# Optimization experiments

Measured on AMD Instinct MI355X. Metric: run time of the kernel, lower is better.

The kernel has to match this reference:

```python
import jax, jax.numpy as jnp
import numpy as np

B, T, S = 4, 4096, 4096
D_MODEL = 512        # d_query = d_value_in = d_key_in
N_HEADS = 8
D_KEY = 512
D_VALUE = 512
N_OMEGA = 64
EPS = 1e-9
DK_H = D_KEY // N_HEADS      # 64
DV_H = D_VALUE // N_HEADS    # 64


def _glorot(key, shape):
    fan_in, fan_out = shape[-2], shape[-1]
    lim = np.sqrt(6.0 / (fan_in + fan_out))
    return jax.random.uniform(key, shape, jnp.float32, -lim, lim)


def _draw_omega(key, d_feature, n_omega):
    # n_omega == d_feature here -> single orthogonal block scaled by sqrt(d)
    g = jax.random.normal(key, (d_feature, d_feature), jnp.float32)
    q, _ = jnp.linalg.qr(g)
    q = q * jnp.sqrt(jnp.float32(d_feature))
    return q[:n_omega]


def setup_inputs() -> dict:
    key = jax.random.key(0)
    ks = jax.random.split(key, 7)
    return {
        "query": 0.5 * jax.random.normal(ks[0], (B, T, D_MODEL), jnp.float32),
        "value": 0.5 * jax.random.normal(ks[1], (B, S, D_MODEL), jnp.float32),
        "key": 0.5 * jax.random.normal(ks[2], (B, S, D_MODEL), jnp.float32),
        "wq": _glorot(ks[3], (N_HEADS, D_MODEL, DK_H)),
        "wv": _glorot(ks[4], (N_HEADS, D_MODEL, DV_H)),
        "wk": _glorot(ks[5], (N_HEADS, D_MODEL, DK_H)),
        "omega": _draw_omega(ks[6], DK_H, N_OMEGA),
    }


def _phi(x, omega):
    # x: (B,H,T,dk_h) -> (B,H,T,2*n_omega) FAVOR+ positive random features
    square_sum = 0.5 * jnp.sum(x * x, axis=-1, keepdims=True)
    xw = jnp.einsum('bhtk,mk->bhtm', x, omega)
    un = jnp.exp(jnp.concatenate([xw, -xw], axis=-1) - square_sum) + EPS
    return un / jnp.sqrt(jnp.float32(2.0 * N_OMEGA))


def reference(query, value, key, wq, wv, wk, omega):
    q = jnp.einsum('btf,hfk->bhtk', query, wq)   # (B,H,T,dk_h)
    v = jnp.einsum('bsd,hdk->bhsk', value, wv)   # (B,H,S,dv_h)
    k = jnp.einsum('bsf,hfk->bhsk', key, wk)     # (B,H,S,dk_h)
    qp = _phi(q, omega)                          # (B,H,T,2M)
    kp = _phi(k, omega)                          # (B,H,S,2M)
    v1 = jnp.concatenate([v, jnp.ones(v.shape[:-1] + (1,), v.dtype)], axis=-1)
    kv = jnp.einsum('bhsm,bhsd->bhmd', kp, v1)   # (B,H,2M,dv_h+1)
    qkv = jnp.einsum('bhtm,bhmd->bhtd', qp, kv)  # (B,H,T,dv_h+1)
    normalizer = qkv[..., -1:]
    out = qkv[..., :-1] / normalizer
    # faithful to original: plain reshape (B,H,T,dv_h) -> (B,T,D_VALUE), no transpose
    return jnp.reshape(out, (B, T, D_VALUE))
```

## Files before the change

kernel.cpp:

```cpp
#include <hip/hip_runtime.h>

typedef _Float16 half8 __attribute__((ext_vector_type(8)));
typedef _Float16 half4_t __attribute__((ext_vector_type(4)));
typedef short short8 __attribute__((ext_vector_type(8)));
typedef unsigned short u16x4 __attribute__((ext_vector_type(4)));
typedef float f32x4 __attribute__((ext_vector_type(4)));

#define NH 8

__device__ __forceinline__ unsigned short f2bf(float x) {
  union { float f; unsigned u; } v; v.f = x;
  unsigned r = v.u + 0x7FFFu + ((v.u >> 16) & 1u);
  return (unsigned short)(r >> 16);
}

#define DRAIN_BAR()                                  \
  asm volatile("s_waitcnt lgkmcnt(0)" ::: "memory"); \
  __builtin_amdgcn_s_barrier();                      \
  __builtin_amdgcn_sched_barrier(0)

__global__ __launch_bounds__(256) void k0_qk(
    const float* __restrict__ wq, const float* __restrict__ wk,
    const float* __restrict__ omega,
    _Float16* __restrict__ wxq, _Float16* __restrict__ wxk) {
  const int bid = blockIdx.x;
  const int arr = bid >> 7;
  const int h = (bid >> 4) & 7;
  const int ft = (bid >> 1) & 7;
  const int os = bid & 1;
  const int f = threadIdx.x & 63;
  const int w = threadIdx.x >> 6;
  const float* wsrc = (arr ? wk : wq) + ((size_t)h * 512 + ft * 64 + f) * 64;
  float wreg[64];
#pragma unroll
  for (int i = 0; i < 16; ++i) {
    float4 v = *(const float4*)(wsrc + i * 4);
    wreg[i * 4] = v.x; wreg[i * 4 + 1] = v.y; wreg[i * 4 + 2] = v.z; wreg[i * 4 + 3] = v.w;
  }
  _Float16* outp = arr ? wxk : wxq;
  const int k8 = f >> 3, e = f & 7;
#pragma unroll 1
  for (int oo = 0; oo < 8; ++oo) {
    const int o = w * 16 + os * 8 + oo;
    const float* om = omega + o * 64;
    float s = 0.f;
#pragma unroll
    for (int k = 0; k < 64; ++k) s = fmaf(wreg[k], om[k], s);
    outp[((((size_t)h * 8 + ft) * 8 + k8) * 64 + o) * 8 + e] = (_Float16)s;
  }
}

__global__ __launch_bounds__(256) void k0_v(
    const float* __restrict__ wv, _Float16* __restrict__ wvt) {
  int idx = blockIdx.x * 256 + threadIdx.x;
  int h = idx >> 15, o = (idx >> 9) & 63, f = idx & 511;
  float val = wv[((size_t)h * 512 + f) * 64 + o];
  wvt[((((size_t)h * 8 + (f >> 6)) * 8 + ((f >> 3) & 7)) * 64 + o) * 8 + (f & 7)] = (_Float16)val;
}

__global__ __launch_bounds__(512, 1) void fused_kv(
    const float* __restrict__ key, const float* __restrict__ value,
    const _Float16* __restrict__ wxk, const _Float16* __restrict__ wvt,
    float* __restrict__ kvpart) {
  __shared__ __align__(16) _Float16 A[2][128][72];
  __shared__ __align__(16) _Float16 W[2][2][4096];
  __shared__ __align__(16) unsigned short kpT[128][136];
  __shared__ __align__(16) unsigned short vT[64][136];
  const int bid = blockIdx.x;
  const int hp = bid >> 6;
  const int b = (bid >> 4) & 3;
  const int sc = bid & 15;
  const int s0 = sc * 256;
  const int tid = threadIdx.x;
  const int w = tid >> 6;
  const int lane = tid & 63;
  const int g = lane >> 4, c = lane & 15;
  const int hh = w >> 2;
  const int rq = w & 3;
  const int xr = lane >> 4;
  const int xc = (lane & 15) * 4;

  const _Float16* wkb0 = wxk + (size_t)(hp * 2) * 32768;
  const _Float16* wkb1 = wkb0 + 32768;
  const _Float16* wvb0 = wvt + (size_t)(hp * 2) * 32768;
  const _Float16* wvb1 = wvb0 + 32768;

  short8 bones;
#pragma unroll
  for (int i = 0; i < 8; ++i) bones[i] = (c == 0) ? (short)0x3F80 : (short)0;

  f32x4 acc_kv[2][5];
#pragma unroll
  for (int h2 = 0; h2 < 2; ++h2)
#pragma unroll
    for (int j = 0; j < 5; ++j) acc_kv[h2][j] = (f32x4){0.f, 0.f, 0.f, 0.f};

  u16x4 kps[2][4], kms[2][4], vs_[2][4];

  float4 xv[4];
  half8 wr0, wr1;

#pragma unroll 1
  for (int p = 0; p < 4; ++p) {
    const float* xb = ((p & 1) ? value : key) +
                      (size_t)(b * 4096 + s0 + (p >> 1) * 128 + w * 16 + xr) * 512 + xc;
    const _Float16* wb0 = (p & 1) ? wvb0 : wkb0;
    const _Float16* wb1 = (p & 1) ? wvb1 : wkb1;

#pragma unroll
    for (int i = 0; i < 4; ++i) xv[i] = *(const float4*)(xb + i * 2048);
    wr0 = *(const half8*)(wb0 + tid * 8);
    wr1 = *(const half8*)(wb1 + tid * 8);
#pragma unroll
    for (int i = 0; i < 4; ++i) {
      float vv[4] = {xv[i].x, xv[i].y, xv[i].z, xv[i].w};
      half4_t hv;
#pragma unroll
      for (int j2 = 0; j2 < 4; ++j2) hv[j2] = (_Float16)vv[j2];
      *(half4_t*)&A[0][w * 16 + i * 4 + xr][xc] = hv;
    }
    *(half8*)&W[0][0][tid * 8] = wr0;
    *(half8*)&W[0][1][tid * 8] = wr1;
#pragma unroll
    for (int i = 0; i < 4; ++i) xv[i] = *(const float4*)(xb + 64 + i * 2048);
    wr0 = *(const half8*)(wb0 + 4096 + tid * 8);
    wr1 = *(const half8*)(wb1 + 4096 + tid * 8);
    DRAIN_BAR();

    f32x4 accp[2][4];
#pragma unroll
    for (int mf = 0; mf < 2; ++mf)
#pragma unroll
      for (int j = 0; j < 4; ++j) accp[mf][j] = (f32x4){0.f, 0.f, 0.f, 0.f};

#pragma unroll 1
    for (int kc = 0; kc < 8; ++kc) {
      const int cur = kc & 1;
      if (kc < 7) {
        const int nxt = cur ^ 1;
#pragma unroll
        for (int i = 0; i < 4; ++i) {
          float vv[4] = {xv[i].x, xv[i].y, xv[i].z, xv[i].w};
          half4_t hv;
#pragma unroll
          for (int j2 = 0; j2 < 4; ++j2) hv[j2] = (_Float16)vv[j2];
          *(half4_t*)&A[nxt][w * 16 + i * 4 + xr][xc] = hv;
        }
        *(half8*)&W[nxt][0][tid * 8] = wr0;
        *(half8*)&W[nxt][1][tid * 8] = wr1;
        if (kc < 6) {
#pragma unroll
          for (int i = 0; i < 4; ++i)
            xv[i] = *(const float4*)(xb + (kc + 2) * 64 + i * 2048);
          wr0 = *(const half8*)(wb0 + (kc + 2) * 4096 + tid * 8);
          wr1 = *(const half8*)(wb1 + (kc + 2) * 4096 + tid * 8);
        }
      }
#pragma unroll
      for (int ks = 0; ks < 2; ++ks) {
        half8 af0 = *(const half8*)&A[cur][rq * 32 + c][ks * 32 + g * 8];
        half8 af1 = *(const half8*)&A[cur][rq * 32 + 16 + c][ks * 32 + g * 8];
#pragma unroll
        for (int nf = 0; nf < 4; ++nf) {
          half8 wf = *(const half8*)&W[cur][hh][((ks * 4 + g) * 64 + nf * 16 + c) * 8];
          accp[0][nf] = __builtin_amdgcn_mfma_f32_16x16x32_f16(af0, wf, accp[0][nf], 0, 0, 0);
          accp[1][nf] = __builtin_amdgcn_mfma_f32_16x16x32_f16(af1, wf, accp[1][nf], 0, 0, 0);
        }
      }
      DRAIN_BAR();
    }

    if ((p & 1) == 0) {
#pragma unroll
      for (int mf = 0; mf < 2; ++mf) {
        float ss_[4];
#pragma unroll
        for (int j = 0; j < 4; ++j) {
          float s = 0.f;
#pragma unroll
          for (int nf = 0; nf < 4; ++nf) { float q = accp[mf][nf][j]; s = fmaf(q, q, s); }
          s += __shfl_xor(s, 1); s += __shfl_xor(s, 2);
          s += __shfl_xor(s, 4); s += __shfl_xor(s, 8);
          ss_[j] = s * 0.0078125f;
        }
#pragma unroll
        for (int nf = 0; nf < 4; ++nf) {
          u16x4 kp_p, kp_m;
#pragma unroll
          for (int j = 0; j < 4; ++j) {
            float v = accp[mf][nf][j];
            kp_p[j] = f2bf(__expf(v - ss_[j]) + 1e-9f);
            kp_m[j] = f2bf(__expf(-v - ss_[j]) + 1e-9f);
          }
          kps[mf][nf] = kp_p;
          kms[mf][nf] = kp_m;
        }
      }
    } else {
#pragma unroll
      for (int mf = 0; mf < 2; ++mf)
#pragma unroll
        for (int nf = 0; nf < 4; ++nf) {
          u16x4 vv;
#pragma unroll
          for (int j = 0; j < 4; ++j) vv[j] = f2bf(accp[mf][nf][j]);
          vs_[mf][nf] = vv;
        }
#pragma unroll
      for (int h2 = 0; h2 < 2; ++h2) {
        if (hh == h2) {
#pragma unroll
          for (int mf = 0; mf < 2; ++mf)
#pragma unroll
            for (int nf = 0; nf < 4; ++nf) {
              const int m = nf * 16 + c;
              const int sl = rq * 32 + mf * 16 + g * 4;
              *(u16x4*)&kpT[m][sl] = kps[mf][nf];
              *(u16x4*)&kpT[64 + m][sl] = kms[mf][nf];
              *(u16x4*)&vT[m][sl] = vs_[mf][nf];
            }
        }
        DRAIN_BAR();
#pragma unroll
        for (int ks = 0; ks < 4; ++ks) {
          short8 a = *(const short8*)&kpT[w * 16 + c][ks * 32 + g * 8];
#pragma unroll
          for (int nf = 0; nf < 4; ++nf) {
            short8 bb = *(const short8*)&vT[nf * 16 + c][ks * 32 + g * 8];
            acc_kv[h2][nf] = __builtin_amdgcn_mfma_f32_16x16x32_bf16(a, bb, acc_kv[h2][nf], 0, 0, 0);
          }
          acc_kv[h2][4] = __builtin_amdgcn_mfma_f32_16x16x32_bf16(a, bones, acc_kv[h2][4], 0, 0, 0);
        }
        __builtin_amdgcn_s_barrier();
      }
    }
  }

#pragma unroll
  for (int h2 = 0; h2 < 2; ++h2) {
    float* pbase = kvpart + ((size_t)sc * 32 + b * 8 + hp * 2 + h2) * 10240;
#pragma unroll
    for (int nf = 0; nf < 5; ++nf)
#pragma unroll
      for (int j = 0; j < 4; ++j)
        pbase[(w * 16 + g * 4 + j) * 80 + nf * 16 + c] = acc_kv[h2][nf][j];
  }
}

__global__ __launch_bounds__(128) void k3a_denom(
    const float* __restrict__ kvpart, float* __restrict__ invbuf,
    float* __restrict__ lsc) {
  const int bh = blockIdx.x;
  const int m = threadIdx.x;
  const float* base = kvpart + (size_t)bh * 10240 + m * 80 + 64;
  float s = 0.f;
#pragma unroll
  for (int kk = 0; kk < 16; ++kk) s += base[(size_t)kk * 327680];
  invbuf[bh * 128 + m] = 1.0f / s;
  lsc[bh * 128 + m] = __logf(s);
}

__global__ __launch_bounds__(256) void k3b_reduce(
    const float* __restrict__ kvpart, const float* __restrict__ invbuf,
    _Float16* __restrict__ kvnt) {
  const int bh = blockIdx.x;
  const int e0 = blockIdx.y * 1024 + threadIdx.x * 4;
  const int m = e0 / 80;
  const int d0 = e0 - m * 80;
  const float* base = kvpart + (size_t)bh * 10240 + e0;
  f32x4 s = (f32x4){0.f, 0.f, 0.f, 0.f};
#pragma unroll
  for (int kk = 0; kk < 16; ++kk) {
    f32x4 v = *(const f32x4*)(base + (size_t)kk * 327680);
    s += v;
  }
  const float inv = invbuf[bh * 128 + m];
  const int mst = ((m & 63) << 1) | (m >> 6);
  _Float16* outb = kvnt + (size_t)bh * 10240 + mst;
#pragma unroll
  for (int j = 0; j < 4; ++j) {
    const int d = d0 + j;
    float val;
    if (d < 64) val = s[j] * inv;
    else if (d == 64) val = 1.0f;
    else val = 0.f;
    outb[d * 128] = (_Float16)val;
  }
}

__global__ __launch_bounds__(256, 4) void fused_qo(
    const float* __restrict__ query, const _Float16* __restrict__ wxq,
    const _Float16* __restrict__ kvnt, const float* __restrict__ lsc,
    float* __restrict__ out) {
  __shared__ __align__(16) _Float16 A[64][72];
  __shared__ __align__(16) _Float16 W[4096];
  __shared__ __align__(16) _Float16 qpT[64][136];
  const int bid = blockIdx.x;
  const int h = bid >> 8;
  const int rt = bid & 255;
  const int R0 = rt * 64;
  const int b = R0 >> 12;
  const int t0 = R0 & 4095;
  const int bh = b * NH + h;
  const int tid = threadIdx.x;
  const int w = tid >> 6;
  const int lane = tid & 63;
  const int g = lane >> 4, c = lane & 15;
  const int srow = tid >> 2;
  const int scol = (tid & 3) * 16;

  const float* xb = query + (size_t)(R0 + srow) * 512 + scol;
  const _Float16* wb = wxq + (size_t)h * 32768;

  float4 xv[4];
  half8 wr0, wr1;
#pragma unroll
  for (int i = 0; i < 4; ++i) xv[i] = *(const float4*)(xb + i * 4);
  wr0 = *(const half8*)(wb + tid * 8);
  wr1 = *(const half8*)(wb + 2048 + tid * 8);

  f32x4 accp[4];
#pragma unroll
  for (int j = 0; j < 4; ++j) accp[j] = (f32x4){0.f, 0.f, 0.f, 0.f};

#pragma unroll 1
  for (int kc = 0; kc < 8; ++kc) {
    DRAIN_BAR();
#pragma unroll
    for (int i = 0; i < 4; ++i) {
      float vv[4] = {xv[i].x, xv[i].y, xv[i].z, xv[i].w};
      half4_t hv;
#pragma unroll
      for (int j2 = 0; j2 < 4; ++j2) hv[j2] = (_Float16)vv[j2];
      *(half4_t*)&A[srow][scol + i * 4] = hv;
    }
    *(half8*)&W[tid * 8] = wr0;
    *(half8*)&W[2048 + tid * 8] = wr1;
    if (kc < 7) {
#pragma unroll
      for (int i = 0; i < 4; ++i)
        xv[i] = *(const float4*)(xb + (kc + 1) * 64 + i * 4);
      wr0 = *(const half8*)(wb + (size_t)(kc + 1) * 4096 + tid * 8);
      wr1 = *(const half8*)(wb + (size_t)(kc + 1) * 4096 + 2048 + tid * 8);
    }
    DRAIN_BAR();
#pragma unroll
    for (int ks = 0; ks < 2; ++ks) {
      half8 a = *(const half8*)&A[w * 16 + c][ks * 32 + g * 8];
#pragma unroll
      for (int nf = 0; nf < 4; ++nf) {
        half8 wf = *(const half8*)&W[((ks * 4 + g) * 64 + nf * 16 + c) * 8];
        accp[nf] = __builtin_amdgcn_mfma_f32_16x16x32_f16(a, wf, accp[nf], 0, 0, 0);
      }
    }
  }

  float Lp[4], Lm[4];
#pragma unroll
  for (int nf = 0; nf < 4; ++nf) {
    Lp[nf] = lsc[bh * 128 + nf * 16 + c];
    Lm[nf] = lsc[bh * 128 + 64 + nf * 16 + c];
  }
  float ss_[4], cm_[4];
#pragma unroll
  for (int j = 0; j < 4; ++j) {
    float s = 0.f;
#pragma unroll
    for (int nf = 0; nf < 4; ++nf) { float q = accp[nf][j]; s = fmaf(q, q, s); }
    s += __shfl_xor(s, 1); s += __shfl_xor(s, 2);
    s += __shfl_xor(s, 4); s += __shfl_xor(s, 8);
    ss_[j] = s * 0.0078125f;
  }
#pragma unroll
  for (int j = 0; j < 4; ++j) {
    float m0 = -1e30f;
#pragma unroll
    for (int nf = 0; nf < 4; ++nf) {
      float v = accp[nf][j];
      m0 = fmaxf(m0, fmaxf(v - ss_[j] + Lp[nf], -v - ss_[j] + Lm[nf]));
      m0 = fmaxf(m0, fmaxf(Lp[nf], Lm[nf]) - 20.723265f);
    }
    m0 = fmaxf(m0, __shfl_xor(m0, 1)); m0 = fmaxf(m0, __shfl_xor(m0, 2));
    m0 = fmaxf(m0, __shfl_xor(m0, 4)); m0 = fmaxf(m0, __shfl_xor(m0, 8));
    cm_[j] = m0;
  }
#pragma unroll
  for (int nf = 0; nf < 4; ++nf) {
    const int m = nf * 16 + c;
#pragma unroll
    for (int j = 0; j < 4; ++j) {
      float v = accp[nf][j];
      _Float16 pp = (_Float16)(__expf(v - ss_[j] + Lp[nf] - cm_[j]) +
                               1e-9f * __expf(Lp[nf] - cm_[j]));
      _Float16 pm = (_Float16)(__expf(-v - ss_[j] + Lm[nf] - cm_[j]) +
                               1e-9f * __expf(Lm[nf] - cm_[j]));
      union { unsigned u; _Float16 hh[2]; } pk;
      pk.hh[0] = pp; pk.hh[1] = pm;
      *(unsigned*)&qpT[w * 16 + g * 4 + j][2 * m] = pk.u;
    }
  }
  DRAIN_BAR();

  f32x4 acco[5];
#pragma unroll
  for (int j = 0; j < 5; ++j) acco[j] = (f32x4){0.f, 0.f, 0.f, 0.f};
  const _Float16* kvb = kvnt + (size_t)bh * 10240;
#pragma unroll
  for (int ks = 0; ks < 4; ++ks) {
    half8 a = *(const half8*)&qpT[w * 16 + c][ks * 32 + g * 8];
#pragma unroll
    for (int nf = 0; nf < 5; ++nf) {
      half8 bb = *(const half8*)(kvb + (size_t)(nf * 16 + c) * 128 + ks * 32 + g * 8);
      acco[nf] = __builtin_amdgcn_mfma_f32_16x16x32_f16(a, bb, acco[nf], 0, 0, 0);
    }
  }
  const int tb = t0 + w * 16 + g * 4;
#pragma unroll
  for (int j = 0; j < 4; ++j) {
    float nrm = __shfl(acco[4][j], (lane & 48));
    float invn = 1.0f / nrm;
#pragma unroll
    for (int nf = 0; nf < 4; ++nf) {
      out[((size_t)bh * 4096 + tb + j) * 64 + nf * 16 + c] = acco[nf][j] * invn;
    }
  }
}

extern "C" void kernel_launch(void* const* d_in, const int* in_sizes, int n_in,
                              void* d_out, int out_size, void* d_ws, size_t ws_size,
                              hipStream_t stream) {
  const float* query = (const float*)d_in[0];
  const float* value = (const float*)d_in[1];
  const float* key   = (const float*)d_in[2];
  const float* wq    = (const float*)d_in[3];
  const float* wv    = (const float*)d_in[4];
  const float* wk    = (const float*)d_in[5];
  const float* omega = (const float*)d_in[6];
  float* out = (float*)d_out;
  char* ws = (char*)d_ws;

  _Float16* wxq  = (_Float16*)(ws);
  _Float16* wxk  = (_Float16*)(ws + 524288);
  _Float16* wvt  = (_Float16*)(ws + 1048576);
  float* kvpart  = (float*)(ws + 1572864);
  _Float16* kvnt = (_Float16*)(ws + 22544384);
  float* lsc     = (float*)(ws + 23199744);
  float* invbuf  = (float*)(ws + 23216128);

  k0_qk<<<256, 256, 0, stream>>>(wq, wk, omega, wxq, wxk);
  k0_v<<<1024, 256, 0, stream>>>(wv, wvt);
  fused_kv<<<256, 512, 0, stream>>>(key, value, wxk, wvt, kvpart);
  k3a_denom<<<32, 128, 0, stream>>>(kvpart, invbuf, lsc);
  k3b_reduce<<<dim3(32, 10), 256, 0, stream>>>(kvpart, invbuf, kvnt);
  fused_qo<<<2048, 256, 0, stream>>>(query, wxq, kvnt, lsc, out);
}
```

Measured before the change: 110.0 us.

## Process four heads per query tile in fused_qo to reuse query loads

Each fused_qo block now computes projections, feature maps and outputs for four heads of one 64-row query tile, so each query tile is read from global memory and converted to fp16 once instead of once per head. The full 256-column half of the query row block is staged in LDS, and projection-weight slices are double-buffered in LDS with register prefetch. The grid shrinks from 2048 to 512 blocks and occupancy is relaxed to 2 blocks per CU. The trade-off is less parallelism, more serial work per block, more LDS per block, and synchronous (non-prefetched) query loads for most of each tile.

```diff
diff --git a/kernel.cpp b/kernel.cpp
--- a/kernel.cpp
+++ b/kernel.cpp
@@ -288,141 +288,189 @@
   }
 }
 
-__global__ __launch_bounds__(256, 4) void fused_qo(
+__global__ __launch_bounds__(256, 2) void fused_qo(
     const float* __restrict__ query, const _Float16* __restrict__ wxq,
     const _Float16* __restrict__ kvnt, const float* __restrict__ lsc,
     float* __restrict__ out) {
-  __shared__ __align__(16) _Float16 A[64][72];
-  __shared__ __align__(16) _Float16 W[4096];
+  __shared__ __align__(16) _Float16 A[64][264];
+  __shared__ __align__(16) _Float16 W[2][4096];
   __shared__ __align__(16) _Float16 qpT[64][136];
   const int bid = blockIdx.x;
-  const int h = bid >> 8;
-  const int rt = bid & 255;
-  const int R0 = rt * 64;
-  const int b = R0 >> 12;
-  const int t0 = R0 & 4095;
-  const int bh = b * NH + h;
+  const int hh2 = bid >> 8;
+  const int b = (bid >> 6) & 3;
+  const int tt = bid & 63;
+  const int t0 = tt * 64;
   const int tid = threadIdx.x;
   const int w = tid >> 6;
   const int lane = tid & 63;
   const int g = lane >> 4, c = lane & 15;
-  const int srow = tid >> 2;
-  const int scol = (tid & 3) * 16;
-
-  const float* xb = query + (size_t)(R0 + srow) * 512 + scol;
-  const _Float16* wb = wxq + (size_t)h * 32768;
+  const int arow = tid >> 2;
+  const int ac4 = (tid & 3) * 16;
+
+  const float* xrow = query + (size_t)(b * 4096 + t0 + arow) * 512 + ac4;
+  const _Float16* wbase = wxq;
+
+  f32x4 accp[4][4];
+#pragma unroll
+  for (int h = 0; h < 4; ++h)
+#pragma unroll
+    for (int j = 0; j < 4; ++j) accp[h][j] = (f32x4){0.f, 0.f, 0.f, 0.f};
 
   float4 xv[4];
   half8 wr0, wr1;
-#pragma unroll
-  for (int i = 0; i < 4; ++i) xv[i] = *(const float4*)(xb + i * 4);
-  wr0 = *(const half8*)(wb + tid * 8);
-  wr1 = *(const half8*)(wb + 2048 + tid * 8);
-
-  f32x4 accp[4];
-#pragma unroll
-  for (int j = 0; j < 4; ++j) accp[j] = (f32x4){0.f, 0.f, 0.f, 0.f};
-
-#pragma unroll 1
-  for (int kc = 0; kc < 8; ++kc) {
+
+#pragma unroll
+  for (int i = 0; i < 4; ++i) xv[i] = *(const float4*)(xrow + i * 64);
+
+#pragma unroll
+  for (int kh = 0; kh < 2; ++kh) {
+#pragma unroll
+    for (int i = 0; i < 4; ++i) {
+      float4 v0 = xv[i];
+      half4_t hv;
+      hv[0] = (_Float16)v0.x; hv[1] = (_Float16)v0.y;
+      hv[2] = (_Float16)v0.z; hv[3] = (_Float16)v0.w;
+      *(half4_t*)&A[arow][ac4 + i * 4] = hv;
+    }
+#pragma unroll
+    for (int i = 0; i < 4; ++i) {
+      float4 v0 = xv[i];
+      half4_t hv;
+      hv[0] = (_Float16)v0.x; hv[1] = (_Float16)v0.y;
+      hv[2] = (_Float16)v0.z; hv[3] = (_Float16)v0.w;
+      *(half4_t*)&A[arow][ac4 + i * 64] = hv;
+    }
+#pragma unroll
+    for (int i = 0; i < 4; ++i) {
+#pragma unroll
+      for (int q2 = 1; q2 < 4; ++q2) {
+        float4 v = *(const float4*)(xrow + kh * 256 + i * 64 + q2 * 4);
+        half4_t hv;
+        hv[0] = (_Float16)v.x; hv[1] = (_Float16)v.y;
+        hv[2] = (_Float16)v.z; hv[3] = (_Float16)v.w;
+        *(half4_t*)&A[arow][ac4 + i * 64 + q2 * 4] = hv;
+      }
+    }
+    {
+      const _Float16* wsl0 = wbase + ((size_t)(hh2 * 4 + 0) * 8 + kh * 4 + 0) * 4096;
+      wr0 = *(const half8*)(wsl0 + tid * 8);
+      wr1 = *(const half8*)(wsl0 + 2048 + tid * 8);
+      *(half8*)&W[0][tid * 8] = wr0;
+      *(half8*)&W[0][2048 + tid * 8] = wr1;
+      const _Float16* wsl1 = wbase + ((size_t)(hh2 * 4 + 0) * 8 + kh * 4 + 1) * 4096;
+      wr0 = *(const half8*)(wsl1 + tid * 8);
+      wr1 = *(const half8*)(wsl1 + 2048 + tid * 8);
+    }
     DRAIN_BAR();
-#pragma unroll
-    for (int i = 0; i < 4; ++i) {
-      float vv[4] = {xv[i].x, xv[i].y, xv[i].z, xv[i].w};
-      half4_t hv;
-#pragma unroll
-      for (int j2 = 0; j2 < 4; ++j2) hv[j2] = (_Float16)vv[j2];
-      *(half4_t*)&A[srow][scol + i * 4] = hv;
-    }
-    *(half8*)&W[tid * 8] = wr0;
-    *(half8*)&W[2048 + tid * 8] = wr1;
-    if (kc < 7) {
-#pragma unroll
-      for (int i = 0; i < 4; ++i)
-        xv[i] = *(const float4*)(xb + (kc + 1) * 64 + i * 4);
-      wr0 = *(const half8*)(wb + (size_t)(kc + 1) * 4096 + tid * 8);
-      wr1 = *(const half8*)(wb + (size_t)(kc + 1) * 4096 + 2048 + tid * 8);
+    if (kh == 0) {
+#pragma unroll
+      for (int i = 0; i < 4; ++i) xv[i] = *(const float4*)(xrow + 256 + i * 64);
+    }
+
+#pragma unroll
+    for (int h = 0; h < 4; ++h) {
+#pragma unroll
+      for (int kc = 0; kc < 4; ++kc) {
+        const int s = h * 4 + kc;
+        const int cur = s & 1;
+        if (s < 15) {
+          *(half8*)&W[cur ^ 1][tid * 8] = wr0;
+          *(half8*)&W[cur ^ 1][2048 + tid * 8] = wr1;
+        }
+        if (s < 14) {
+          const int sn = s + 2;
+          const _Float16* wsl = wbase +
+              ((size_t)(hh2 * 4 + (sn >> 2)) * 8 + kh * 4 + (sn & 3)) * 4096;
+          wr0 = *(const half8*)(wsl + tid * 8);
+          wr1 = *(const half8*)(wsl + 2048 + tid * 8);
+        }
+#pragma unroll
+        for (int ks = 0; ks < 2; ++ks) {
+          half8 a = *(const half8*)&A[w * 16 + c][kc * 64 + ks * 32 + g * 8];
+#pragma unroll
+          for (int nf = 0; nf < 4; ++nf) {
+            half8 wf = *(const half8*)&W[cur][((ks * 4 + g) * 64 + nf * 16 + c) * 8];
+            accp[h][nf] = __builtin_amdgcn_mfma_f32_16x16x32_f16(a, wf, accp[h][nf], 0, 0, 0);
+          }
+        }
+        DRAIN_BAR();
+      }
+    }
+  }
+
+#pragma unroll
+  for (int h = 0; h < 4; ++h) {
+    const int bh = b * NH + hh2 * 4 + h;
+    float Lp[4], Lm[4];
+#pragma unroll
+    for (int nf = 0; nf < 4; ++nf) {
+      Lp[nf] = lsc[bh * 128 + nf * 16 + c];
+      Lm[nf] = lsc[bh * 128 + 64 + nf * 16 + c];
+    }
+    float ss_[4], cm_[4];
+#pragma unroll
+    for (int j = 0; j < 4; ++j) {
+      float s = 0.f;
+#pragma unroll
+      for (int nf = 0; nf < 4; ++nf) { float q = accp[h][nf][j]; s = fmaf(q, q, s); }
+      s += __shfl_xor(s, 1); s += __shfl_xor(s, 2);
+      s += __shfl_xor(s, 4); s += __shfl_xor(s, 8);
+      ss_[j] = s * 0.0078125f;
+    }
+#pragma unroll
+    for (int j = 0; j < 4; ++j) {
+      float m0 = -1e30f;
+#pragma unroll
+      for (int nf = 0; nf < 4; ++nf) {
+        float v = accp[h][nf][j];
+        m0 = fmaxf(m0, fmaxf(v - ss_[j] + Lp[nf], -v - ss_[j] + Lm[nf]));
+        m0 = fmaxf(m0, fmaxf(Lp[nf], Lm[nf]) - 20.723265f);
+      }
+      m0 = fmaxf(m0, __shfl_xor(m0, 1)); m0 = fmaxf(m0, __shfl_xor(m0, 2));
+      m0 = fmaxf(m0, __shfl_xor(m0, 4)); m0 = fmaxf(m0, __shfl_xor(m0, 8));
+      cm_[j] = m0;
+    }
+#pragma unroll
+    for (int nf = 0; nf < 4; ++nf) {
+      const int m = nf * 16 + c;
+#pragma unroll
+      for (int j = 0; j < 4; ++j) {
+        float v = accp[h][nf][j];
+        _Float16 pp = (_Float16)(__expf(v - ss_[j] + Lp[nf] - cm_[j]) +
+                                 1e-9f * __expf(Lp[nf] - cm_[j]));
+        _Float16 pm = (_Float16)(__expf(-v - ss_[j] + Lm[nf] - cm_[j]) +
+                                 1e-9f * __expf(Lm[nf] - cm_[j]));
+        union { unsigned u; _Float16 hh_[2]; } pk;
+        pk.hh_[0] = pp; pk.hh_[1] = pm;
+        *(unsigned*)&qpT[w * 16 + g * 4 + j][2 * m] = pk.u;
+      }
     }
     DRAIN_BAR();
-#pragma unroll
-    for (int ks = 0; ks < 2; ++ks) {
-      half8 a = *(const half8*)&A[w * 16 + c][ks * 32 + g * 8];
+
+    f32x4 acco[5];
+#pragma unroll
+    for (int j = 0; j < 5; ++j) acco[j] = (f32x4){0.f, 0.f, 0.f, 0.f};
+    const _Float16* kvb = kvnt + (size_t)bh * 10240;
+#pragma unroll
+    for (int ks = 0; ks < 4; ++ks) {
+      half8 a = *(const half8*)&qpT[w * 16 + c][ks * 32 + g * 8];
+#pragma unroll
+      for (int nf = 0; nf < 5; ++nf) {
+        half8 bb = *(const half8*)(kvb + (size_t)(nf * 16 + c) * 128 + ks * 32 + g * 8);
+        acco[nf] = __builtin_amdgcn_mfma_f32_16x16x32_f16(a, bb, acco[nf], 0, 0, 0);
+      }
+    }
+    const int tb = t0 + w * 16 + g * 4;
+#pragma unroll
+    for (int j = 0; j < 4; ++j) {
+      float nrm = __shfl(acco[4][j], (lane & 48));
+      float invn = 1.0f / nrm;
 #pragma unroll
       for (int nf = 0; nf < 4; ++nf) {
-        half8 wf = *(const half8*)&W[((ks * 4 + g) * 64 + nf * 16 + c) * 8];
-        accp[nf] = __builtin_amdgcn_mfma_f32_16x16x32_f16(a, wf, accp[nf], 0, 0, 0);
-      }
-    }
-  }
-
-  float Lp[4], Lm[4];
-#pragma unroll
-  for (int nf = 0; nf < 4; ++nf) {
-    Lp[nf] = lsc[bh * 128 + nf * 16 + c];
-    Lm[nf] = lsc[bh * 128 + 64 + nf * 16 + c];
-  }
-  float ss_[4], cm_[4];
-#pragma unroll
-  for (int j = 0; j < 4; ++j) {
-    float s = 0.f;
-#pragma unroll
-    for (int nf = 0; nf < 4; ++nf) { float q = accp[nf][j]; s = fmaf(q, q, s); }
-    s += __shfl_xor(s, 1); s += __shfl_xor(s, 2);
-    s += __shfl_xor(s, 4); s += __shfl_xor(s, 8);
-    ss_[j] = s * 0.0078125f;
-  }
-#pragma unroll
-  for (int j = 0; j < 4; ++j) {
-    float m0 = -1e30f;
-#pragma unroll
-    for (int nf = 0; nf < 4; ++nf) {
-      float v = accp[nf][j];
-      m0 = fmaxf(m0, fmaxf(v - ss_[j] + Lp[nf], -v - ss_[j] + Lm[nf]));
-      m0 = fmaxf(m0, fmaxf(Lp[nf], Lm[nf]) - 20.723265f);
-    }
-    m0 = fmaxf(m0, __shfl_xor(m0, 1)); m0 = fmaxf(m0, __shfl_xor(m0, 2));
-    m0 = fmaxf(m0, __shfl_xor(m0, 4)); m0 = fmaxf(m0, __shfl_xor(m0, 8));
-    cm_[j] = m0;
-  }
-#pragma unroll
-  for (int nf = 0; nf < 4; ++nf) {
-    const int m = nf * 16 + c;
-#pragma unroll
-    for (int j = 0; j < 4; ++j) {
-      float v = accp[nf][j];
-      _Float16 pp = (_Float16)(__expf(v - ss_[j] + Lp[nf] - cm_[j]) +
-                               1e-9f * __expf(Lp[nf] - cm_[j]));
-      _Float16 pm = (_Float16)(__expf(-v - ss_[j] + Lm[nf] - cm_[j]) +
-                               1e-9f * __expf(Lm[nf] - cm_[j]));
-      union { unsigned u; _Float16 hh[2]; } pk;
-      pk.hh[0] = pp; pk.hh[1] = pm;
-      *(unsigned*)&qpT[w * 16 + g * 4 + j][2 * m] = pk.u;
-    }
-  }
-  DRAIN_BAR();
-
-  f32x4 acco[5];
-#pragma unroll
-  for (int j = 0; j < 5; ++j) acco[j] = (f32x4){0.f, 0.f, 0.f, 0.f};
-  const _Float16* kvb = kvnt + (size_t)bh * 10240;
-#pragma unroll
-  for (int ks = 0; ks < 4; ++ks) {
-    half8 a = *(const half8*)&qpT[w * 16 + c][ks * 32 + g * 8];
-#pragma unroll
-    for (int nf = 0; nf < 5; ++nf) {
-      half8 bb = *(const half8*)(kvb + (size_t)(nf * 16 + c) * 128 + ks * 32 + g * 8);
-      acco[nf] = __builtin_amdgcn_mfma_f32_16x16x32_f16(a, bb, acco[nf], 0, 0, 0);
-    }
-  }
-  const int tb = t0 + w * 16 + g * 4;
-#pragma unroll
-  for (int j = 0; j < 4; ++j) {
-    float nrm = __shfl(acco[4][j], (lane & 48));
-    float invn = 1.0f / nrm;
-#pragma unroll
-    for (int nf = 0; nf < 4; ++nf) {
-      out[((size_t)bh * 4096 + tb + j) * 64 + nf * 16 + c] = acco[nf][j] * invn;
-    }
+        out[((size_t)bh * 4096 + tb + j) * 64 + nf * 16 + c] = acco[nf][j] * invn;
+      }
+    }
+    DRAIN_BAR();
   }
 }
 
@@ -452,5 +500,5 @@
   fused_kv<<<256, 512, 0, stream>>>(key, value, wxk, wvt, kvpart);
   k3a_denom<<<32, 128, 0, stream>>>(kvpart, invbuf, lsc);
   k3b_reduce<<<dim3(32, 10), 256, 0, stream>>>(kvpart, invbuf, kvnt);
-  fused_qo<<<2048, 256, 0, stream>>>(query, wxq, kvnt, lsc, out);
-}
+  fused_qo<<<512, 256, 0, stream>>>(query, wxq, kvnt, lsc, out);
+}
```

Result: no change. 111.3 us (+1.2%).
